# Performance work log

Hardware: AMD Instinct MI355X
Metric: run time of the kernel (lower is better)

The kernel has to match this reference:

```python
import jax, jax.numpy as jnp
import numpy as np

B, NQ, DM = 2, 8192, 256
NH, DH, NL, NP = 6, 64, 3, 9
IMG_H, IMG_W = 384, 1280
SHAPES = [(48, 160), (24, 80), (12, 40)]  # (h, w) per pyramid level


def setup_inputs() -> dict:
    key = jax.random.key(0)
    ks = jax.random.split(key, 16)
    inp = {}
    inp["x"] = jax.random.normal(ks[0], (B, NQ, DM), jnp.float32)
    inp["pe"] = jax.random.normal(ks[1], (B, NQ, DM), jnp.float32)
    # lidar points in front of the camera so projected uv mostly lands in-image
    u = jax.random.uniform(ks[2], (B, NQ, 3), jnp.float32)
    inp["coor"] = jnp.stack([(u[..., 0] - 0.5) * 40.0,
                             (u[..., 1] - 0.5) * 4.0,
                             2.0 + u[..., 2] * 48.0], axis=-1)
    K = jnp.array([[700., 0., 640., 0.], [0., 700., 192., 0.],
                   [0., 0., 1., 0.], [0., 0., 0., 1.]], jnp.float32)
    inp["cam2img"] = jnp.broadcast_to(K, (B, 4, 4))
    inp["lidar2cam"] = jnp.broadcast_to(jnp.eye(4, dtype=jnp.float32), (B, 4, 4))
    for i, (h, w) in enumerate(SHAPES):
        inp[f"feat{i}"] = jax.random.normal(ks[3 + i], (B, DM, h, w), jnp.float32) * 0.1
    s = 1.0 / np.sqrt(DM).astype(np.float32)
    inp["W_value"] = jax.random.normal(ks[6], (DM, NH * DH), jnp.float32) * s
    inp["b_value"] = jnp.zeros((NH * DH,), jnp.float32)
    inp["W_off"] = jax.random.normal(ks[7], (DM, NH * NL * NP * 2), jnp.float32) * 0.01
    inp["b_off"] = jax.random.normal(ks[8], (NH * NL * NP * 2,), jnp.float32)
    inp["W_attn"] = jax.random.normal(ks[9], (DM, NH * NL * NP), jnp.float32) * s
    inp["b_attn"] = jnp.zeros((NH * NL * NP,), jnp.float32)
    inp["W_out"] = jax.random.normal(ks[10], (NH * DH, DM), jnp.float32) * (1.0 / np.sqrt(NH * DH)).astype(np.float32)
    inp["b_out"] = jnp.zeros((DM,), jnp.float32)
    return inp


def _points2uv(points, cam2img, lidar2cam):
    R, t = lidar2cam[:, :3, :3], lidar2cam[:, :3, 3]
    pc = jnp.einsum('bij,bnj->bni', R, points) + t[:, None, :]
    Kr, Kt = cam2img[:, :3, :3], cam2img[:, :3, 3]
    p2 = jnp.einsum('bij,bnj->bni', Kr, pc) + Kt[:, None, :]
    return p2[..., :2] / p2[..., 2:3]  # [B,NQ,2] (u,v)


def _bilinear_gather(v, loc, hl, wl):
    # v: [B*NH, hl*wl, DH] values; loc: [B,NQ,NH,NP,2] normalized [0,1]
    # matches grid_sample(bilinear, padding=zeros, align_corners=False)
    x = loc[..., 0] * wl - 0.5
    y = loc[..., 1] * hl - 0.5
    x0 = jnp.floor(x)
    y0 = jnp.floor(y)
    fx = x - x0
    fy = y - y0
    acc = jnp.zeros((B, NH, NQ, NP, DH), v.dtype)
    for dy in (0, 1):
        for dx in (0, 1):
            xi = x0 + dx
            yi = y0 + dy
            wgt = (fx if dx else 1.0 - fx) * (fy if dy else 1.0 - fy)
            valid = (xi >= 0) & (xi < wl) & (yi >= 0) & (yi < hl)
            idx = (jnp.clip(yi, 0, hl - 1) * wl + jnp.clip(xi, 0, wl - 1)).astype(jnp.int32)
            idx = idx.transpose(0, 2, 1, 3).reshape(B * NH, NQ * NP)
            g = jax.vmap(lambda vt, it: vt[it])(v, idx)  # [B*NH, NQ*NP, DH]
            g = g.reshape(B, NH, NQ, NP, DH)
            wv = (wgt * valid).transpose(0, 2, 1, 3)      # [B,NH,NQ,NP]
            acc = acc + g * wv[..., None]
    return acc


def reference(x, pe, coor, cam2img, lidar2cam, feat0, feat1, feat2,
              W_value, b_value, W_off, b_off, W_attn, b_attn, W_out, b_out):
    feats = [feat0, feat1, feat2]
    uv = _points2uv(coor, cam2img, lidar2cam)  # [B,NQ,2]
    # per-level reference points in level pixel coords: uv * (w_l/W, h_l/H)
    ref = jnp.stack([uv * jnp.array([w / IMG_W, h / IMG_H], jnp.float32)
                     for (h, w) in SHAPES], axis=2)  # [B,NQ,NL,2]
    q = x + pe
    off = (q @ W_off + b_off).reshape(B, NQ, NH, NL, NP, 2)
    attn = jax.nn.softmax((q @ W_attn + b_attn).reshape(B, NQ, NH, NL * NP), axis=-1)
    attn = attn.reshape(B, NQ, NH, NL, NP).transpose(0, 2, 1, 3, 4)  # [B,NH,NQ,NL,NP]
    norm = jnp.array([[w, h] for (h, w) in SHAPES], jnp.float32)     # [NL,2] (w,h)
    loc = (ref[:, :, None, :, None, :] + off) / norm[None, None, None, :, None, :]
    out = jnp.zeros((B, NH, NQ, DH), jnp.float32)
    for l, (h, w) in enumerate(SHAPES):
        src = feats[l].reshape(B, DM, h * w).transpose(0, 2, 1)  # [B,hw,DM]
        v = (src @ W_value + b_value).reshape(B, h * w, NH, DH)
        v = v.transpose(0, 2, 1, 3).reshape(B * NH, h * w, DH)
        sampled = _bilinear_gather(v, loc[:, :, :, l], h, w)    # [B,NH,NQ,NP,DH]
        out = out + jnp.einsum('bhqp,bhqpd->bhqd', attn[:, :, :, l], sampled)
    out = out.transpose(0, 2, 1, 3).reshape(B, NQ, NH * DH)
    return out @ W_out + b_out  # dropout is identity at eval
```

## Files before the change

kernel.cpp:

```cpp
#include <hip/hip_runtime.h>
#include <hip/hip_bf16.h>

#define NQ_   8192
#define DM_   256
#define NH_   6
#define DH_   64
#define BATCH 2

typedef __attribute__((ext_vector_type(8))) short short8;
typedef __attribute__((ext_vector_type(4))) short short4v;
typedef __attribute__((ext_vector_type(4))) float float4v;
typedef __attribute__((ext_vector_type(2))) float f32x2;

static const size_t VOFF_L0 = 0;
static const size_t VOFF_L1 = 5898240;
static const size_t VOFF_L2 = 7372800;
static const size_t QRAW_BYTE_OFF  = 15482880;
static const size_t MID_BYTE_OFF   = 47333376;
static const size_t QBF_BYTE_OFF   = 47333376;
static const size_t WT_BYTE_OFF    = 59916288;
static const size_t FEATT_BYTE_OFF = 60558336;
static const size_t WVT_OFF   = 0;
static const size_t WOFFT_OFF = 98304;
static const size_t WOUTT_OFF = 222720;
static const size_t FT_L0 = 0;
static const size_t FT_L1 = 3932160;
static const size_t FT_L2 = 4915200;

__device__ __forceinline__ unsigned short f2bf(float f) {
    unsigned int u = __float_as_uint(f);
    unsigned int r = (u + 0x7fffu + ((u >> 16) & 1u)) >> 16;
    return (unsigned short)r;
}

__device__ __forceinline__ void cp16(void* lds, const void* g) {
    __builtin_amdgcn_global_load_lds(
        (const __attribute__((address_space(1))) unsigned int*)g,
        (__attribute__((address_space(3))) unsigned int*)lds, 16, 0, 0);
}

__global__ __launch_bounds__(256) void prep_all(const float* __restrict__ Wv,
                                                const float* __restrict__ Woff,
                                                const float* __restrict__ Wattn,
                                                const float* __restrict__ Wout,
                                                const float* __restrict__ feat0,
                                                const float* __restrict__ feat1,
                                                const float* __restrict__ feat2,
                                                const float* __restrict__ x,
                                                const float* __restrict__ pe,
                                                unsigned short* __restrict__ wT,
                                                unsigned short* __restrict__ fT,
                                                unsigned short* __restrict__ qbf) {
    const int pid = blockIdx.x, t = threadIdx.x;
    if (pid < 1126) {
        int r = pid;
        const float* src; int N, n, K; size_t doff;
        if (r < 384)      { src = Wv;    N = 384; n = r;       K = 256; doff = (size_t)r * 256; }
        else if (r < 708) { src = Woff;  N = 324; n = r - 384; K = 256; doff = (size_t)r * 256; }
        else if (r < 870) { src = Wattn; N = 162; n = r - 708; K = 256; doff = (size_t)r * 256; }
        else              { src = Wout;  N = 256; n = r - 870; K = 384; doff = WOUTT_OFF + (size_t)(r - 870) * 384; }
        for (int k = t; k < K; k += 256) wT[doff + k] = f2bf(src[(size_t)k * N + n]);
        return;
    }
    if (pid < 3646) {
        __shared__ float tile[64][33];
        int f = pid - 1126;
        const float* src; unsigned short* dst; int HW;
        if (f < 1920)      { src = feat0; dst = fT + FT_L0; HW = 7680; }
        else if (f < 2400) { src = feat1; dst = fT + FT_L1; HW = 1920; f -= 1920; }
        else               { src = feat2; dst = fT + FT_L2; HW = 480;  f -= 2400; }
        int pb = f >> 3, rem = f & 7, cb = rem >> 1, b = rem & 1;
        int p0 = pb * 32, c0 = cb * 64;
        {
            int px = t & 31, cy = t >> 5;
#pragma unroll
            for (int i = 0; i < 8; ++i) {
                int cr = cy + i * 8;
                tile[cr][px] = src[((size_t)(b * DM_ + c0 + cr)) * HW + p0 + px];
            }
        }
        __syncthreads();
        {
            int cx = t & 63, py = t >> 6;
#pragma unroll
            for (int i = 0; i < 8; ++i) {
                int pr = py + i * 4;
                dst[((size_t)b * HW + p0 + pr) * DM_ + c0 + cx] = f2bf(tile[cx][pr]);
            }
        }
        return;
    }
    int f = pid - 3646;
#pragma unroll
    for (int i = 0; i < 4; ++i) {
        size_t e = (size_t)f * 4096 + i * 1024 + t * 4;
        float4 xv = *(const float4*)&x[e];
        float4 pv = *(const float4*)&pe[e];
        short4v o;
        o[0] = (short)f2bf(xv.x + pv.x);
        o[1] = (short)f2bf(xv.y + pv.y);
        o[2] = (short)f2bf(xv.z + pv.z);
        o[3] = (short)f2bf(xv.w + pv.w);
        *(short4v*)&qbf[e] = o;
    }
}

__device__ __forceinline__ void mfma_block32(const short A[][32], const short B[][32],
                                             int wm, int wn, int lane, float4v acc[4][4]) {
    int m_base = wm + (lane & 15);
    int n_base = wn + (lane & 15);
    int q8 = (lane >> 4) * 8;
    short8 af[4], bf[4];
#pragma unroll
    for (int i = 0; i < 4; ++i) af[i] = *(const short8*)&A[m_base + i * 16][q8];
#pragma unroll
    for (int j = 0; j < 4; ++j) bf[j] = *(const short8*)&B[n_base + j * 16][q8];
#pragma unroll
    for (int i = 0; i < 4; ++i)
#pragma unroll
        for (int j = 0; j < 4; ++j)
            acc[i][j] = __builtin_amdgcn_mfma_f32_16x16x32_bf16(af[i], bf[j], acc[i][j], 0, 0, 0);
}

__global__ __launch_bounds__(256) void gemm_vq(const unsigned short* __restrict__ fT,
                                               const unsigned short* __restrict__ wT,
                                               const float* __restrict__ bv,
                                               unsigned short* __restrict__ vws,
                                               const unsigned short* __restrict__ qbf,
                                               const float* __restrict__ boff,
                                               const float* __restrict__ battn,
                                               float* __restrict__ qraw) {
    __shared__ short A[128][32];
    __shared__ short B[128][32];
    const int tid = threadIdx.x;
    const int lane = tid & 63, wave = tid >> 6;
    const int wm = (wave & 1) * 64, wn = (wave >> 1) * 64;
    const int id = blockIdx.x;
    const int r0 = tid >> 2, sg8 = (tid & 3) * 8;
    float4v acc[4][4];
#pragma unroll
    for (int i = 0; i < 4; ++i)
#pragma unroll
        for (int j = 0; j < 4; ++j) acc[i][j] = (float4v){0.f, 0.f, 0.f, 0.f};

    if (id < 474) {
        int pb = id / 6, rem = id % 6;
        int nb = rem >> 1, b = rem & 1;
        int pbl, HW; size_t ftoff, voff;
        if (pb < 60)      { pbl = pb;      HW = 7680; ftoff = FT_L0; voff = VOFF_L0; }
        else if (pb < 75) { pbl = pb - 60; HW = 1920; ftoff = FT_L1; voff = VOFF_L1; }
        else              { pbl = pb - 75; HW = 480;  ftoff = FT_L2; voff = VOFF_L2; }
        const int p0 = pbl * 128, n0 = nb * 128;
        const unsigned short* Asrc = fT + ftoff + (size_t)b * HW * DM_;
        const unsigned short* wvT = wT + WVT_OFF;
        int p1 = p0 + r0;      if (p1 >= HW) p1 = HW - 1;
        int p2 = p0 + r0 + 64; if (p2 >= HW) p2 = HW - 1;

        for (int k0 = 0; k0 < DM_; k0 += 32) {
            cp16(&A[r0][sg8],      &Asrc[(size_t)p1 * DM_ + k0 + sg8]);
            cp16(&A[r0 + 64][sg8], &Asrc[(size_t)p2 * DM_ + k0 + sg8]);
            cp16(&B[r0][sg8],      &wvT[(size_t)(n0 + r0) * DM_ + k0 + sg8]);
            cp16(&B[r0 + 64][sg8], &wvT[(size_t)(n0 + r0 + 64) * DM_ + k0 + sg8]);
            __syncthreads();
            mfma_block32(A, B, wm, wn, lane, acc);
            __syncthreads();
        }
        int colb = n0 + wn + (lane & 15);
        int rowq = (lane >> 4) * 4;
#pragma unroll
        for (int i = 0; i < 4; ++i)
#pragma unroll
            for (int j = 0; j < 4; ++j) {
                int n = colb + j * 16;
                int h = n >> 6, d = n & 63;
                float bias = bv[n];
#pragma unroll
                for (int r = 0; r < 4; ++r) {
                    int p = p0 + wm + i * 16 + rowq + r;
                    if (p < HW)
                        vws[voff + ((size_t)(b * NH_ + h) * HW + p) * DH_ + d] = f2bf(acc[i][j][r] + bias);
                }
            }
    } else {
        int qid = id - 474;
        const int m0 = (qid & 127) * 128, n0 = (qid >> 7) * 128;
        const unsigned short* wq = wT + WOFFT_OFF;

        for (int k0 = 0; k0 < DM_; k0 += 32) {
            cp16(&A[r0][sg8],      &qbf[(size_t)(m0 + r0) * DM_ + k0 + sg8]);
            cp16(&A[r0 + 64][sg8], &qbf[(size_t)(m0 + r0 + 64) * DM_ + k0 + sg8]);
            cp16(&B[r0][sg8],      &wq[(size_t)(n0 + r0) * DM_ + k0 + sg8]);
            cp16(&B[r0 + 64][sg8], &wq[(size_t)(n0 + r0 + 64) * DM_ + k0 + sg8]);
            __syncthreads();
            mfma_block32(A, B, wm, wn, lane, acc);
            __syncthreads();
        }
        int colb = n0 + wn + (lane & 15);
        int rowq = (lane >> 4) * 4;
#pragma unroll
        for (int i = 0; i < 4; ++i)
#pragma unroll
            for (int j = 0; j < 4; ++j) {
                int n = colb + j * 16;
                if (n < 486) {
                    float bias = (n < 324) ? boff[n] : battn[n - 324];
#pragma unroll
                    for (int r = 0; r < 4; ++r) {
                        int m = m0 + wm + i * 16 + rowq + r;
                        qraw[(size_t)m * 486 + n] = acc[i][j][r] + bias;
                    }
                }
            }
    }
}

__global__ __launch_bounds__(384, 5) void sample_kernel(const float* __restrict__ qraw,
                                                        const float* __restrict__ coor,
                                                        const float* __restrict__ cam2img,
                                                        const float* __restrict__ l2c,
                                                        const unsigned short* __restrict__ vws,
                                                        unsigned short* __restrict__ mid) {
    __shared__ int2 s_plan[1416];
    const int tid = threadIdx.x;
    const int bq0 = blockIdx.x * 2;

    {
        int q = tid >= 192;
        int t = tid - q * 192;
        int bq = bq0 + q;
        int b = bq >> 13;
        int h = t >> 5, j = t & 31;
        bool act = j < 27;
        float logit = act ? qraw[(size_t)bq * 486 + 324 + h * 27 + j] : -1e30f;
        float m = logit;
#pragma unroll
        for (int msk = 16; msk >= 1; msk >>= 1) m = fmaxf(m, __shfl_xor(m, msk, 32));
        float e = act ? __expf(logit - m) : 0.f;
        float ssum = e;
#pragma unroll
        for (int msk = 16; msk >= 1; msk >>= 1) ssum += __shfl_xor(ssum, msk, 32);
        if (act) {
            float attn = e * __frcp_rn(ssum);
            int l = (j >= 18) ? 2 : ((j >= 9) ? 1 : 0);
            int wl = 160 >> l, hl = 48 >> l;
            int HWl = (l == 0) ? 7680 : ((l == 1) ? 1920 : 480);
            int lvlb = (l == 0) ? 0 : ((l == 1) ? 11796480 : 14745600);
            float sc = (l == 0) ? 0.125f : ((l == 1) ? 0.0625f : 0.03125f);
            float c0 = coor[(size_t)bq * 3 + 0];
            float c1 = coor[(size_t)bq * 3 + 1];
            float c2 = coor[(size_t)bq * 3 + 2];
            const float* L = l2c + b * 16;
            const float* C = cam2img + b * 16;
            float pc0 = L[0] * c0 + L[1] * c1 + L[2]  * c2 + L[3];
            float pc1 = L[4] * c0 + L[5] * c1 + L[6]  * c2 + L[7];
            float pc2 = L[8] * c0 + L[9] * c1 + L[10] * c2 + L[11];
            float q0 = C[0] * pc0 + C[1] * pc1 + C[2]  * pc2 + C[3];
            float q1 = C[4] * pc0 + C[5] * pc1 + C[6]  * pc2 + C[7];
            float q2 = C[8] * pc0 + C[9] * pc1 + C[10] * pc2 + C[11];
            float rz = __frcp_rn(q2);
            float refx = q0 * rz * sc, refy = q1 * rz * sc;
            float2 oxy = *(const float2*)&qraw[(size_t)bq * 486 + h * 54 + j * 2];
            float X = refx + oxy.x - 0.5f;
            float Y = refy + oxy.y - 0.5f;
            float x0f = floorf(X), y0f = floorf(Y);
            float fx = X - x0f, fy = Y - y0f;
            int ix = (int)x0f, iy = (int)y0f;
            int bx = min(max(ix, 0), wl - 2);
            float wx0 = ((bx == ix) ? (1.f - fx) : 0.f) + ((bx == ix + 1) ? fx : 0.f);
            float wx1 = ((bx + 1 == ix) ? (1.f - fx) : 0.f) + ((bx + 1 == ix + 1) ? fx : 0.f);
            int cy0 = min(max(iy, 0), hl - 1);
            int cy1 = min(max(iy + 1, 0), hl - 1);
            float wy0 = (iy >= 0 && iy < hl) ? (1.f - fy) : 0.f;
            float wy1 = (iy + 1 >= 0 && iy + 1 < hl) ? fy : 0.f;
            int jj = h * 27 + j;
            int slice = (b * NH_ + h) * HWl;
            int off0 = lvlb + (slice + cy0 * wl + bx) * 128;
            int off1 = lvlb + (slice + cy1 * wl + bx) * 128;
            int pb = q * 4 * 177 + jj;
            s_plan[pb]           = make_int2(off0,       __float_as_int(attn * wy0 * wx0));
            s_plan[pb + 177]     = make_int2(off0 + 128, __float_as_int(attn * wy0 * wx1));
            s_plan[pb + 2 * 177] = make_int2(off1,       __float_as_int(attn * wy1 * wx0));
            s_plan[pb + 3 * 177] = make_int2(off1 + 128, __float_as_int(attn * wy1 * wx1));
        }
    }
    __syncthreads();

    const int h = tid >> 6;
    const int lane = tid & 63;
    const int plane = lane >> 3;
    const unsigned cb = (unsigned)((lane & 7) << 4);
    const char* vbase = (const char*)vws;
    const int2* pl = &s_plan[plane * 177 + h * 27];
    f32x2 A0 = {0.f, 0.f}, A1 = {0.f, 0.f}, A2 = {0.f, 0.f}, A3 = {0.f, 0.f};

    int g0 = 0;
#pragma unroll
    for (int g = 0; g < 5; ++g) {
        const int N = (g < 4) ? 6 : 3;
        int2 pw[6];
        uint4 d[6];
#pragma unroll
        for (int t = 0; t < N; ++t) pw[t] = pl[g0 + t];
#pragma unroll
        for (int t = 0; t < N; ++t) d[t] = *(const uint4*)(vbase + ((unsigned)pw[t].x + cb));
#pragma unroll
        for (int t = 0; t < N; ++t) {
            float w = __int_as_float(pw[t].y);
            f32x2 w2 = {w, w};
            f32x2 v0 = {__uint_as_float(d[t].x << 16), __uint_as_float(d[t].x & 0xffff0000u)};
            f32x2 v1 = {__uint_as_float(d[t].y << 16), __uint_as_float(d[t].y & 0xffff0000u)};
            f32x2 v2 = {__uint_as_float(d[t].z << 16), __uint_as_float(d[t].z & 0xffff0000u)};
            f32x2 v3 = {__uint_as_float(d[t].w << 16), __uint_as_float(d[t].w & 0xffff0000u)};
            A0 = __builtin_elementwise_fma(w2, v0, A0);
            A1 = __builtin_elementwise_fma(w2, v1, A1);
            A2 = __builtin_elementwise_fma(w2, v2, A2);
            A3 = __builtin_elementwise_fma(w2, v3, A3);
        }
        g0 += N;
    }

    float a[8] = {A0.x, A0.y, A1.x, A1.y, A2.x, A2.y, A3.x, A3.y};
#pragma unroll
    for (int i = 0; i < 8; ++i) {
        a[i] += __shfl_xor(a[i], 8, 64);
        a[i] += __shfl_xor(a[i], 16, 64);
    }
    if (((lane >> 3) & 3) == 0) {
        int q = lane >> 5;
        uint4 pk;
        pk.x = (unsigned)f2bf(a[0]) | ((unsigned)f2bf(a[1]) << 16);
        pk.y = (unsigned)f2bf(a[2]) | ((unsigned)f2bf(a[3]) << 16);
        pk.z = (unsigned)f2bf(a[4]) | ((unsigned)f2bf(a[5]) << 16);
        pk.w = (unsigned)f2bf(a[6]) | ((unsigned)f2bf(a[7]) << 16);
        *(uint4*)&mid[(size_t)(bq0 + q) * 384 + h * DH_ + ((lane & 7) << 3)] = pk;
    }
}

__global__ __launch_bounds__(256) void out_gemm(const unsigned short* __restrict__ mid,
                                                const unsigned short* __restrict__ woT,
                                                const float* __restrict__ bout,
                                                float* __restrict__ out) {
    __shared__ short A[64][32];
    __shared__ short B[128][32];
    const int tid = threadIdx.x;
    const int m0 = blockIdx.x * 64, n0 = blockIdx.y * 128;
    const int lane = tid & 63, wave = tid >> 6;
    const int wn = wave * 32;
    const int r0 = tid >> 2, sg8 = (tid & 3) * 8;
    float4v acc[4][2];
#pragma unroll
    for (int i = 0; i < 4; ++i)
#pragma unroll
        for (int j = 0; j < 2; ++j) acc[i][j] = (float4v){0.f, 0.f, 0.f, 0.f};

    for (int k0 = 0; k0 < 384; k0 += 32) {
        cp16(&A[r0][sg8],      &mid[(size_t)(m0 + r0) * 384 + k0 + sg8]);
        cp16(&B[r0][sg8],      &woT[(size_t)(n0 + r0) * 384 + k0 + sg8]);
        cp16(&B[r0 + 64][sg8], &woT[(size_t)(n0 + r0 + 64) * 384 + k0 + sg8]);
        __syncthreads();
        {
            int m_base = lane & 15;
            int n_base = wn + (lane & 15);
            int q8 = (lane >> 4) * 8;
            short8 af[4], bf[2];
#pragma unroll
            for (int i = 0; i < 4; ++i) af[i] = *(const short8*)&A[m_base + i * 16][q8];
#pragma unroll
            for (int j = 0; j < 2; ++j) bf[j] = *(const short8*)&B[n_base + j * 16][q8];
#pragma unroll
            for (int i = 0; i < 4; ++i)
#pragma unroll
                for (int j = 0; j < 2; ++j)
                    acc[i][j] = __builtin_amdgcn_mfma_f32_16x16x32_bf16(af[i], bf[j], acc[i][j], 0, 0, 0);
        }
        __syncthreads();
    }
    int colb = n0 + wn + (lane & 15);
    int rowq = (lane >> 4) * 4;
#pragma unroll
    for (int i = 0; i < 4; ++i)
#pragma unroll
        for (int j = 0; j < 2; ++j) {
            int n = colb + j * 16;
            float bias = bout[n];
#pragma unroll
            for (int r = 0; r < 4; ++r) {
                int m = m0 + i * 16 + rowq + r;
                out[(size_t)m * 256 + n] = acc[i][j][r] + bias;
            }
        }
}

extern "C" void kernel_launch(void* const* d_in, const int* in_sizes, int n_in,
                              void* d_out, int out_size, void* d_ws, size_t ws_size,
                              hipStream_t stream) {
    const float* x      = (const float*)d_in[0];
    const float* pe     = (const float*)d_in[1];
    const float* coor   = (const float*)d_in[2];
    const float* c2i    = (const float*)d_in[3];
    const float* l2c    = (const float*)d_in[4];
    const float* feat0  = (const float*)d_in[5];
    const float* feat1  = (const float*)d_in[6];
    const float* feat2  = (const float*)d_in[7];
    const float* Wv     = (const float*)d_in[8];
    const float* bv     = (const float*)d_in[9];
    const float* Woff   = (const float*)d_in[10];
    const float* boff   = (const float*)d_in[11];
    const float* Wattn  = (const float*)d_in[12];
    const float* battn  = (const float*)d_in[13];
    const float* Wout   = (const float*)d_in[14];
    const float* bout   = (const float*)d_in[15];

    unsigned short* vws = (unsigned short*)d_ws;
    float* qraw         = (float*)((char*)d_ws + QRAW_BYTE_OFF);
    unsigned short* mid = (unsigned short*)((char*)d_ws + MID_BYTE_OFF);
    unsigned short* qbf = (unsigned short*)((char*)d_ws + QBF_BYTE_OFF);
    unsigned short* wT  = (unsigned short*)((char*)d_ws + WT_BYTE_OFF);
    unsigned short* fT  = (unsigned short*)((char*)d_ws + FEATT_BYTE_OFF);
    float* out          = (float*)d_out;

    prep_all<<<dim3(4670), 256, 0, stream>>>(Wv, Woff, Wattn, Wout, feat0, feat1, feat2,
                                             x, pe, wT, fT, qbf);
    gemm_vq<<<dim3(986), 256, 0, stream>>>(fT, wT, bv, vws, qbf, boff, battn, qraw);
    sample_kernel<<<dim3(BATCH * NQ_ / 2), 384, 0, stream>>>(qraw, coor, c2i, l2c, vws, mid);
    out_gemm<<<dim3(256, 2), 256, 0, stream>>>(mid, wT + WOUTT_OFF, bout, out);
}
```

Baseline: 215.3 us.

## Sort queries by projected level-0 cell to improve sampling locality

Adds a counting sort that projects each lidar point to image space, buckets queries by their level-0 reference pixel, and builds a permutation. The sampling kernel then processes queries in this spatially sorted order, so neighbouring blocks gather overlapping value rows and cache reuse should improve. It costs a memset plus three small kernels, one of them a single-block scan, and the scattered reads of qraw and writes of mid by permuted index.

```diff
diff --git a/kernel.cpp b/kernel.cpp
--- a/kernel.cpp
+++ b/kernel.cpp
@@ -20,6 +20,9 @@
 static const size_t QBF_BYTE_OFF   = 47333376;
 static const size_t WT_BYTE_OFF    = 59916288;
 static const size_t FEATT_BYTE_OFF = 60558336;
+static const size_t KEYS_BYTE_OFF  = 70880256;
+static const size_t CNT_BYTE_OFF   = 70945792;
+static const size_t PERM_BYTE_OFF  = 71007232;
 static const size_t WVT_OFF   = 0;
 static const size_t WOFFT_OFF = 98304;
 static const size_t WOUTT_OFF = 222720;
@@ -105,6 +108,62 @@
     }
 }
 
+__global__ __launch_bounds__(256) void sort_keys(const float* __restrict__ coor,
+                                                 const float* __restrict__ cam2img,
+                                                 const float* __restrict__ l2c,
+                                                 int* __restrict__ keys,
+                                                 int* __restrict__ cnt) {
+    int q = blockIdx.x * 256 + threadIdx.x;
+    int b = q >> 13;
+    float c0 = coor[(size_t)q * 3 + 0];
+    float c1 = coor[(size_t)q * 3 + 1];
+    float c2 = coor[(size_t)q * 3 + 2];
+    const float* L = l2c + b * 16;
+    const float* C = cam2img + b * 16;
+    float pc0 = L[0] * c0 + L[1] * c1 + L[2]  * c2 + L[3];
+    float pc1 = L[4] * c0 + L[5] * c1 + L[6]  * c2 + L[7];
+    float pc2 = L[8] * c0 + L[9] * c1 + L[10] * c2 + L[11];
+    float q0 = C[0] * pc0 + C[1] * pc1 + C[2]  * pc2 + C[3];
+    float q1 = C[4] * pc0 + C[5] * pc1 + C[6]  * pc2 + C[7];
+    float q2 = C[8] * pc0 + C[9] * pc1 + C[10] * pc2 + C[11];
+    float rz = __frcp_rn(q2);
+    float refx = q0 * rz * 0.125f, refy = q1 * rz * 0.125f;
+    int cx = min(max((int)floorf(refx), 0), 159);
+    int cy = min(max((int)floorf(refy), 0), 47);
+    int key = b * 7680 + cy * 160 + cx;
+    keys[q] = key;
+    atomicAdd(&cnt[key], 1);
+}
+
+__global__ __launch_bounds__(256) void scan_offsets(int* __restrict__ cnt) {
+    __shared__ int buf[15360];
+    __shared__ int part[256];
+    int t = threadIdx.x;
+    for (int i = t; i < 15360; i += 256) buf[i] = cnt[i];
+    __syncthreads();
+    int base = t * 60, s = 0;
+#pragma unroll 4
+    for (int i = 0; i < 60; ++i) { int v = buf[base + i]; buf[base + i] = s; s += v; }
+    part[t] = s;
+    __syncthreads();
+    if (t == 0) {
+        int s2 = 0;
+        for (int i = 0; i < 256; ++i) { int v = part[i]; part[i] = s2; s2 += v; }
+    }
+    __syncthreads();
+    int add = part[t];
+#pragma unroll 4
+    for (int i = 0; i < 60; ++i) cnt[base + i] = buf[base + i] + add;
+}
+
+__global__ __launch_bounds__(256) void scatter_perm(const int* __restrict__ keys,
+                                                    int* __restrict__ cnt,
+                                                    int* __restrict__ perm) {
+    int q = blockIdx.x * 256 + threadIdx.x;
+    int pos = atomicAdd(&cnt[keys[q]], 1);
+    perm[pos] = q;
+}
+
 __device__ __forceinline__ void mfma_block32(const short A[][32], const short B[][32],
                                              int wm, int wn, int lane, float4v acc[4][4]) {
     int m_base = wm + (lane & 15);
@@ -219,15 +278,17 @@
                                                         const float* __restrict__ cam2img,
                                                         const float* __restrict__ l2c,
                                                         const unsigned short* __restrict__ vws,
+                                                        const int* __restrict__ perm,
                                                         unsigned short* __restrict__ mid) {
     __shared__ int2 s_plan[1416];
+    __shared__ int s_bq[2];
     const int tid = threadIdx.x;
-    const int bq0 = blockIdx.x * 2;
 
     {
         int q = tid >= 192;
         int t = tid - q * 192;
-        int bq = bq0 + q;
+        int bq = perm[blockIdx.x * 2 + q];
+        if (t == 0) s_bq[q] = bq;
         int b = bq >> 13;
         int h = t >> 5, j = t & 31;
         bool act = j < 27;
@@ -327,12 +388,13 @@
     }
     if (((lane >> 3) & 3) == 0) {
         int q = lane >> 5;
+        int bqw = s_bq[q];
         uint4 pk;
         pk.x = (unsigned)f2bf(a[0]) | ((unsigned)f2bf(a[1]) << 16);
         pk.y = (unsigned)f2bf(a[2]) | ((unsigned)f2bf(a[3]) << 16);
         pk.z = (unsigned)f2bf(a[4]) | ((unsigned)f2bf(a[5]) << 16);
         pk.w = (unsigned)f2bf(a[6]) | ((unsigned)f2bf(a[7]) << 16);
-        *(uint4*)&mid[(size_t)(bq0 + q) * 384 + h * DH_ + ((lane & 7) << 3)] = pk;
+        *(uint4*)&mid[(size_t)bqw * 384 + h * DH_ + ((lane & 7) << 3)] = pk;
     }
 }
 
@@ -417,11 +479,18 @@
     unsigned short* qbf = (unsigned short*)((char*)d_ws + QBF_BYTE_OFF);
     unsigned short* wT  = (unsigned short*)((char*)d_ws + WT_BYTE_OFF);
     unsigned short* fT  = (unsigned short*)((char*)d_ws + FEATT_BYTE_OFF);
+    int* keys           = (int*)((char*)d_ws + KEYS_BYTE_OFF);
+    int* cnt            = (int*)((char*)d_ws + CNT_BYTE_OFF);
+    int* perm           = (int*)((char*)d_ws + PERM_BYTE_OFF);
     float* out          = (float*)d_out;
 
+    hipMemsetAsync(cnt, 0, 15360 * sizeof(int), stream);
+    sort_keys<<<dim3(64), 256, 0, stream>>>(coor, c2i, l2c, keys, cnt);
+    scan_offsets<<<dim3(1), 256, 0, stream>>>(cnt);
+    scatter_perm<<<dim3(64), 256, 0, stream>>>(keys, cnt, perm);
     prep_all<<<dim3(4670), 256, 0, stream>>>(Wv, Woff, Wattn, Wout, feat0, feat1, feat2,
                                              x, pe, wT, fT, qbf);
     gemm_vq<<<dim3(986), 256, 0, stream>>>(fT, wT, bv, vws, qbf, boff, battn, qraw);
-    sample_kernel<<<dim3(BATCH * NQ_ / 2), 384, 0, stream>>>(qraw, coor, c2i, l2c, vws, mid);
+    sample_kernel<<<dim3(BATCH * NQ_ / 2), 384, 0, stream>>>(qraw, coor, c2i, l2c, vws, perm, mid);
     out_gemm<<<dim3(256, 2), 256, 0, stream>>>(mid, wT + WOUTT_OFF, bout, out);
 }
```

Result: slower. 241.9 us (+12.4%).
